# Kernel tuning notes

Measured on AMD Instinct MI355X. Metric: run time of the kernel, lower is better.

The kernel has to match this reference:

```python
import jax, jax.numpy as jnp
import numpy as np

QUALITY = 95
X_MIN, X_MAX = 0.0, 1.0

# JPEG Annex K base quantization tables
_LUMA = np.array([
    [16, 11, 10, 16, 24, 40, 51, 61],
    [12, 12, 14, 19, 26, 58, 60, 55],
    [14, 13, 16, 24, 40, 57, 69, 56],
    [14, 17, 22, 29, 51, 87, 80, 62],
    [18, 22, 37, 56, 68, 109, 103, 77],
    [24, 35, 55, 64, 81, 104, 113, 92],
    [49, 64, 78, 87, 103, 121, 120, 101],
    [72, 92, 95, 98, 112, 100, 103, 99]], dtype=np.float32)
_CHROMA = np.array([
    [17, 18, 24, 47, 99, 99, 99, 99],
    [18, 21, 26, 66, 99, 99, 99, 99],
    [24, 26, 56, 99, 99, 99, 99, 99],
    [47, 66, 99, 99, 99, 99, 99, 99],
    [99, 99, 99, 99, 99, 99, 99, 99],
    [99, 99, 99, 99, 99, 99, 99, 99],
    [99, 99, 99, 99, 99, 99, 99, 99],
    [99, 99, 99, 99, 99, 99, 99, 99]], dtype=np.float32)

def _qtable(base, quality):
    # libjpeg quality scaling (quality >= 50 branch)
    scale = 5000.0 / quality if quality < 50 else 200.0 - 2.0 * quality
    return np.clip(np.floor((base * scale + 50.0) / 100.0), 1.0, 255.0).astype(np.float32)

_QL = jnp.asarray(_qtable(_LUMA, QUALITY))
_QC = jnp.asarray(_qtable(_CHROMA, QUALITY))

# Orthonormal 8x8 DCT-II matrix
_k = np.arange(8)
_D = np.sqrt(2.0 / 8.0) * np.cos((2 * _k[None, :] + 1) * _k[:, None] * np.pi / 16.0)
_D[0, :] /= np.sqrt(2.0)
_D = jnp.asarray(_D.astype(np.float32))

def _jpeg_channel(ch, table):
    """8x8 block DCT -> quantize(round) -> dequantize -> IDCT. ch: [B,H,W] level-shifted."""
    B, H, W = ch.shape
    xb = ch.reshape(B, H // 8, 8, W // 8, 8)
    coef = jnp.einsum('ki,bhiwj,lj->bhkwl', _D, xb, _D)
    t = table[None, None, :, None, :]
    deq = jnp.round(coef / t) * t
    rec = jnp.einsum('ki,bhkwl,lj->bhiwj', _D, deq, _D)
    return rec.reshape(B, H, W)

def _jpeg_roundtrip(x255):
    """x255: [B,H,W,3] float values in [0,255]. Simulates JPEG encode+decode (4:2:0)."""
    r, g, b = x255[..., 0], x255[..., 1], x255[..., 2]
    # JFIF RGB -> YCbCr
    y = 0.299 * r + 0.587 * g + 0.114 * b
    cb = -0.168736 * r - 0.331264 * g + 0.5 * b + 128.0
    cr = 0.5 * r - 0.418688 * g - 0.081312 * b + 128.0
    # Luma at full resolution
    y2 = _jpeg_channel(y - 128.0, _QL) + 128.0
    # Chroma: 2x2 average downsample (4:2:0), codec, nearest upsample
    def down(c):
        B, H, W = c.shape
        return c.reshape(B, H // 2, 2, W // 2, 2).mean(axis=(2, 4))
    def up(c):
        return jnp.repeat(jnp.repeat(c, 2, axis=1), 2, axis=2)
    cb2 = up(_jpeg_channel(down(cb) - 128.0, _QC) + 128.0)
    cr2 = up(_jpeg_channel(down(cr) - 128.0, _QC) + 128.0)
    # YCbCr -> RGB
    r2 = y2 + 1.402 * (cr2 - 128.0)
    g2 = y2 - 0.344136 * (cb2 - 128.0) - 0.714136 * (cr2 - 128.0)
    b2 = y2 + 1.772 * (cb2 - 128.0)
    rgb = jnp.stack([r2, g2, b2], axis=-1)
    return jnp.round(jnp.clip(rgb, 0.0, 255.0))  # decoded uint8 values


def setup_inputs() -> dict:
    key = jax.random.key(0)
    x = jax.random.uniform(key, (32, 512, 512, 3), dtype=jnp.float32)
    return {"x": x}


def reference(x):
    # inputs -> uint8 pixel values (tf.cast truncation; values are >= 0)
    x255 = jnp.clip(jnp.floor((x - X_MIN) / ((X_MAX - X_MIN) / 255.0)), 0.0, 255.0)
    dec = _jpeg_roundtrip(x255)
    # back to input range/dtype
    return dec / (255.0 / (X_MAX - X_MIN)) + X_MIN
```

## Files before the change

### kernel.cpp

```cpp
#include <hip/hip_runtime.h>
#include <cstddef>

static constexpr float D8[8][8] = {
  { 0.35355339059327373f, 0.35355339059327373f, 0.35355339059327373f, 0.35355339059327373f,
    0.35355339059327373f, 0.35355339059327373f, 0.35355339059327373f, 0.35355339059327373f},
  { 0.4903926402016152f,  0.4157348061512726f,  0.27778511650980114f, 0.09754516100806417f,
   -0.09754516100806417f,-0.27778511650980114f,-0.4157348061512726f, -0.4903926402016152f},
  { 0.46193976625564337f, 0.19134171618254492f,-0.19134171618254492f,-0.46193976625564337f,
   -0.46193976625564337f,-0.19134171618254492f, 0.19134171618254492f, 0.46193976625564337f},
  { 0.4157348061512726f, -0.09754516100806417f,-0.4903926402016152f, -0.27778511650980114f,
    0.27778511650980114f, 0.4903926402016152f,  0.09754516100806417f,-0.4157348061512726f},
  { 0.35355339059327373f,-0.35355339059327373f,-0.35355339059327373f, 0.35355339059327373f,
    0.35355339059327373f,-0.35355339059327373f,-0.35355339059327373f, 0.35355339059327373f},
  { 0.27778511650980114f,-0.4903926402016152f,  0.09754516100806417f, 0.4157348061512726f,
   -0.4157348061512726f, -0.09754516100806417f, 0.4903926402016152f, -0.27778511650980114f},
  { 0.19134171618254492f,-0.46193976625564337f, 0.46193976625564337f,-0.19134171618254492f,
   -0.19134171618254492f, 0.46193976625564337f,-0.46193976625564337f, 0.19134171618254492f},
  { 0.09754516100806417f,-0.27778511650980114f, 0.4157348061512726f, -0.4903926402016152f,
    0.4903926402016152f, -0.4157348061512726f,  0.27778511650980114f,-0.09754516100806417f},
};

static constexpr float QLt[8][8] = {
  {2,1,1,2,2,4,5,6},
  {1,1,1,2,3,6,6,6},
  {1,1,2,2,4,6,7,6},
  {1,2,2,3,5,9,8,6},
  {2,2,4,6,7,11,10,8},
  {2,4,6,6,8,10,11,9},
  {5,6,8,9,10,12,12,10},
  {7,9,10,10,11,10,10,10},
};
static constexpr float QCt[8][8] = {
  {2,2,2,5,10,10,10,10},
  {2,2,3,7,10,10,10,10},
  {2,3,6,10,10,10,10,10},
  {5,7,10,10,10,10,10,10},
  {10,10,10,10,10,10,10,10},
  {10,10,10,10,10,10,10,10},
  {10,10,10,10,10,10,10,10},
  {10,10,10,10,10,10,10,10},
};

static constexpr float C255  = (float)(1.0/255.0);
static constexpr float RC255 = 1.0f / C255;

__device__ __forceinline__ float exact_div(float x, float c, float r) {
  float q0 = x * r;
  float e  = fmaf(-c, q0, x);
  return fmaf(e, r, q0);
}

__device__ __forceinline__ void dct8(const float x[8], float u[8]) {
  #pragma unroll
  for (int k = 0; k < 8; ++k) {
    float a = D8[k][0] * x[0];
    #pragma unroll
    for (int j = 1; j < 8; ++j) a += D8[k][j] * x[j];
    u[k] = a;
  }
}

__device__ __forceinline__ void idct8(const float x[8], float u[8]) {
  #pragma unroll
  for (int j = 0; j < 8; ++j) {
    float a = x[0] * D8[0][j];
    #pragma unroll
    for (int m = 1; m < 8; ++m) a += x[m] * D8[m][j];
    u[j] = a;
  }
}

__device__ __forceinline__ void xpose3(float a[8], float b[8], float c[8], int lane) {
  #pragma unroll
  for (int s = 1; s < 8; s <<= 1) {
    const bool hi = (lane & s) != 0;
    #pragma unroll
    for (int r0 = 0; r0 < 8; ++r0) {
      if (r0 & s) continue;
      const int r1 = r0 | s;
      const float a0 = a[r0], a1 = a[r1];
      const float b0 = b[r0], b1 = b[r1];
      const float c0 = c[r0], c1 = c[r1];
      const float ga = __shfl_xor(hi ? a0 : a1, s, 64);
      const float gb = __shfl_xor(hi ? b0 : b1, s, 64);
      const float gc = __shfl_xor(hi ? c0 : c1, s, 64);
      a[r0] = hi ? ga : a0;  a[r1] = hi ? a1 : ga;
      b[r0] = hi ? gb : b0;  b[r1] = hi ? b1 : gb;
      c[r0] = hi ? gc : c0;  c[r1] = hi ? c1 : gc;
    }
  }
}

__device__ __forceinline__ void quant8(float v[8], const float* QT, const float* RQ) {
  float4 Q0 = *(const float4*)&QT[0];
  float4 Q1 = *(const float4*)&QT[4];
  float4 R0 = *(const float4*)&RQ[0];
  float4 R1 = *(const float4*)&RQ[4];
  float qv[8] = {Q0.x,Q0.y,Q0.z,Q0.w,Q1.x,Q1.y,Q1.z,Q1.w};
  float rv[8] = {R0.x,R0.y,R0.z,R0.w,R1.x,R1.y,R1.z,R1.w};
  #pragma unroll
  for (int m = 0; m < 8; ++m)
    v[m] = rintf(exact_div(v[m], qv[m], rv[m])) * qv[m];
}

__global__ __launch_bounds__(64, 4) void jpeg_rt(const float* __restrict__ in,
                                                 float* __restrict__ out)
{
  __shared__ __align__(16) float Cbp[8][36];
  __shared__ __align__(16) float Crp[8][36];
  __shared__ __align__(16) float QTs[2][8][8];
  __shared__ __align__(16) float RQs[2][8][8];

  const int t   = threadIdx.x;
  const int g   = t >> 3;
  const int l   = t & 7;
  const int tx  = blockIdx.x;
  const int ty  = blockIdx.y;
  const int img = blockIdx.z;

  {
    const int i = t >> 3, m = t & 7;
    #pragma unroll
    for (int pl = 0; pl < 2; ++pl) {
      const float q = pl ? QCt[m][i] : QLt[m][i];
      QTs[pl][i][m] = q;
      RQs[pl][i][m] = 1.0f / q;
    }
  }

  const size_t imgbase = (size_t)img * (512*512);
  const int col0 = tx*64 + g*8;

  float vA[8], vB[8];

  #pragma unroll
  for (int rr = 0; rr < 2; ++rr) {
    const int r = l + rr*8;
    const float* rp = in + (imgbase + (size_t)(ty*16 + r)*512 + col0)*3;
    float4 P0 = ((const float4*)rp)[0];
    float4 P1 = ((const float4*)rp)[1];
    float4 P2 = ((const float4*)rp)[2];
    float4 P3 = ((const float4*)rp)[3];
    float4 P4 = ((const float4*)rp)[4];
    float4 P5 = ((const float4*)rp)[5];
    float px[24] = {P0.x,P0.y,P0.z,P0.w,P1.x,P1.y,P1.z,P1.w,
                    P2.x,P2.y,P2.z,P2.w,P3.x,P3.y,P3.z,P3.w,
                    P4.x,P4.y,P4.z,P4.w,P5.x,P5.y,P5.z,P5.w};
    float yv[8], cbv[8], crv[8];
    #pragma unroll
    for (int p = 0; p < 8; ++p) {
      float rc = fminf(fmaxf(floorf(exact_div(px[3*p+0], C255, RC255)), 0.0f), 255.0f);
      float gc = fminf(fmaxf(floorf(exact_div(px[3*p+1], C255, RC255)), 0.0f), 255.0f);
      float bc = fminf(fmaxf(floorf(exact_div(px[3*p+2], C255, RC255)), 0.0f), 255.0f);
      float y  =  0.299f*rc + 0.587f*gc + 0.114f*bc;
      float cb = -0.168736f*rc - 0.331264f*gc + 0.5f*bc + 128.0f;
      float cr =  0.5f*rc - 0.418688f*gc - 0.081312f*bc + 128.0f;
      yv[p]  = y - 128.0f;
      cbv[p] = cb;
      crv[p] = cr;
    }
    float hcb[4], hcr[4];
    #pragma unroll
    for (int k = 0; k < 4; ++k) {
      hcb[k] = cbv[2*k] + cbv[2*k+1];
      hcr[k] = crv[2*k] + crv[2*k+1];
    }
    float ocb[4], ocr[4];
    #pragma unroll
    for (int k = 0; k < 4; ++k) {
      ocb[k] = __shfl_xor(hcb[k], 1, 64);
      ocr[k] = __shfl_xor(hcr[k], 1, 64);
    }
    if ((l & 1) == 0) {
      const int crow = r >> 1;
      *(float4*)&Cbp[crow][g*4] = make_float4(
        (hcb[0]+ocb[0])*0.25f - 128.0f, (hcb[1]+ocb[1])*0.25f - 128.0f,
        (hcb[2]+ocb[2])*0.25f - 128.0f, (hcb[3]+ocb[3])*0.25f - 128.0f);
      *(float4*)&Crp[crow][g*4] = make_float4(
        (hcr[0]+ocr[0])*0.25f - 128.0f, (hcr[1]+ocr[1])*0.25f - 128.0f,
        (hcr[2]+ocr[2])*0.25f - 128.0f, (hcr[3]+ocr[3])*0.25f - 128.0f);
    }
    #pragma unroll
    for (int p = 0; p < 8; ++p) {
      if (rr == 0) vA[p] = yv[p]; else vB[p] = yv[p];
    }
  }
  __syncthreads();

  {
    float* plane = (g & 4) ? &Crp[0][0] : &Cbp[0][0];
    float* rowp  = plane + l*36 + (g & 3)*8;
    float4 L0 = *(const float4*)&rowp[0];
    float4 L1 = *(const float4*)&rowp[4];
    float vC[8] = {L0.x,L0.y,L0.z,L0.w,L1.x,L1.y,L1.z,L1.w};
    float uA[8], uB[8], uC[8];
    dct8(vA, uA); dct8(vB, uB); dct8(vC, uC);
    xpose3(uA, uB, uC, l);
    dct8(uA, vA); quant8(vA, &QTs[0][l][0], &RQs[0][l][0]);
    dct8(uB, vB); quant8(vB, &QTs[0][l][0], &RQs[0][l][0]);
    dct8(uC, vC); quant8(vC, &QTs[1][l][0], &RQs[1][l][0]);
    idct8(vA, uA); idct8(vB, uB); idct8(vC, uC);
    xpose3(uA, uB, uC, l);
    idct8(uA, vA); idct8(uB, vB); idct8(uC, vC);
    *(float4*)&rowp[0] = make_float4(vC[0],vC[1],vC[2],vC[3]);
    *(float4*)&rowp[4] = make_float4(vC[4],vC[5],vC[6],vC[7]);
  }
  __syncthreads();

  #pragma unroll
  for (int rr = 0; rr < 2; ++rr) {
    const int r = l + rr*8;
    const int crow = r >> 1;
    float4 CbF = *(const float4*)&Cbp[crow][g*4];
    float4 CrF = *(const float4*)&Crp[crow][g*4];
    float cbq[4] = {CbF.x,CbF.y,CbF.z,CbF.w};
    float crq[4] = {CrF.x,CrF.y,CrF.z,CrF.w};
    float ov[24];
    #pragma unroll
    for (int p = 0; p < 8; ++p) {
      float y2  = (rr ? vB[p] : vA[p]) + 128.0f;
      float cb2 = cbq[p>>1] + 128.0f;
      float cr2 = crq[p>>1] + 128.0f;
      float r2 = y2 + 1.402f*(cr2 - 128.0f);
      float g2 = y2 - 0.344136f*(cb2 - 128.0f) - 0.714136f*(cr2 - 128.0f);
      float b2 = y2 + 1.772f*(cb2 - 128.0f);
      ov[3*p+0] = exact_div(rintf(fminf(fmaxf(r2, 0.0f), 255.0f)), 255.0f, C255);
      ov[3*p+1] = exact_div(rintf(fminf(fmaxf(g2, 0.0f), 255.0f)), 255.0f, C255);
      ov[3*p+2] = exact_div(rintf(fminf(fmaxf(b2, 0.0f), 255.0f)), 255.0f, C255);
    }
    float* op = out + (imgbase + (size_t)(ty*16 + r)*512 + col0)*3;
    ((float4*)op)[0] = make_float4(ov[0], ov[1], ov[2], ov[3]);
    ((float4*)op)[1] = make_float4(ov[4], ov[5], ov[6], ov[7]);
    ((float4*)op)[2] = make_float4(ov[8], ov[9], ov[10],ov[11]);
    ((float4*)op)[3] = make_float4(ov[12],ov[13],ov[14],ov[15]);
    ((float4*)op)[4] = make_float4(ov[16],ov[17],ov[18],ov[19]);
    ((float4*)op)[5] = make_float4(ov[20],ov[21],ov[22],ov[23]);
  }
}

extern "C" void kernel_launch(void* const* d_in, const int* in_sizes, int n_in,
                              void* d_out, int out_size, void* d_ws, size_t ws_size,
                              hipStream_t stream) {
  (void)in_sizes; (void)n_in; (void)d_ws; (void)ws_size; (void)out_size;
  const float* x = (const float*)d_in[0];
  float* out = (float*)d_out;
  dim3 grid(8, 32, 32);
  jpeg_rt<<<grid, dim3(64), 0, stream>>>(x, out);
}
```

Measured before the change: 191.5 us.

## Process two row tiles per wave with prefetched loads overlapping compute

Each workgroup now has two waves, and each wave handles two 16-row tiles in sequence. The next tile's global row loads are issued before the DCT and output phases of the current tile, so memory latency overlaps compute. Plain __syncthreads is replaced by a raw LDS waitcnt plus s_barrier, and there are 4x fewer blocks. In exchange, the prefetched Row24 values raise register pressure, which may lower occupancy, and there is less block-level parallelism.

```diff
diff --git a/kernel.cpp b/kernel.cpp
--- a/kernel.cpp
+++ b/kernel.cpp
@@ -103,116 +103,81 @@
     v[m] = rintf(exact_div(v[m], qv[m], rv[m])) * qv[m];
 }
 
-__global__ __launch_bounds__(64, 4) void jpeg_rt(const float* __restrict__ in,
-                                                 float* __restrict__ out)
-{
-  __shared__ __align__(16) float Cbp[8][36];
-  __shared__ __align__(16) float Crp[8][36];
-  __shared__ __align__(16) float QTs[2][8][8];
-  __shared__ __align__(16) float RQs[2][8][8];
-
-  const int t   = threadIdx.x;
-  const int g   = t >> 3;
-  const int l   = t & 7;
-  const int tx  = blockIdx.x;
-  const int ty  = blockIdx.y;
-  const int img = blockIdx.z;
-
-  {
-    const int i = t >> 3, m = t & 7;
-    #pragma unroll
-    for (int pl = 0; pl < 2; ++pl) {
-      const float q = pl ? QCt[m][i] : QLt[m][i];
-      QTs[pl][i][m] = q;
-      RQs[pl][i][m] = 1.0f / q;
-    }
-  }
-
-  const size_t imgbase = (size_t)img * (512*512);
-  const int col0 = tx*64 + g*8;
-
-  float vA[8], vB[8];
-
-  #pragma unroll
-  for (int rr = 0; rr < 2; ++rr) {
-    const int r = l + rr*8;
-    const float* rp = in + (imgbase + (size_t)(ty*16 + r)*512 + col0)*3;
-    float4 P0 = ((const float4*)rp)[0];
-    float4 P1 = ((const float4*)rp)[1];
-    float4 P2 = ((const float4*)rp)[2];
-    float4 P3 = ((const float4*)rp)[3];
-    float4 P4 = ((const float4*)rp)[4];
-    float4 P5 = ((const float4*)rp)[5];
-    float px[24] = {P0.x,P0.y,P0.z,P0.w,P1.x,P1.y,P1.z,P1.w,
-                    P2.x,P2.y,P2.z,P2.w,P3.x,P3.y,P3.z,P3.w,
-                    P4.x,P4.y,P4.z,P4.w,P5.x,P5.y,P5.z,P5.w};
-    float yv[8], cbv[8], crv[8];
-    #pragma unroll
-    for (int p = 0; p < 8; ++p) {
-      float rc = fminf(fmaxf(floorf(exact_div(px[3*p+0], C255, RC255)), 0.0f), 255.0f);
-      float gc = fminf(fmaxf(floorf(exact_div(px[3*p+1], C255, RC255)), 0.0f), 255.0f);
-      float bc = fminf(fmaxf(floorf(exact_div(px[3*p+2], C255, RC255)), 0.0f), 255.0f);
-      float y  =  0.299f*rc + 0.587f*gc + 0.114f*bc;
-      float cb = -0.168736f*rc - 0.331264f*gc + 0.5f*bc + 128.0f;
-      float cr =  0.5f*rc - 0.418688f*gc - 0.081312f*bc + 128.0f;
-      yv[p]  = y - 128.0f;
-      cbv[p] = cb;
-      crv[p] = cr;
-    }
-    float hcb[4], hcr[4];
-    #pragma unroll
-    for (int k = 0; k < 4; ++k) {
-      hcb[k] = cbv[2*k] + cbv[2*k+1];
-      hcr[k] = crv[2*k] + crv[2*k+1];
-    }
-    float ocb[4], ocr[4];
-    #pragma unroll
-    for (int k = 0; k < 4; ++k) {
-      ocb[k] = __shfl_xor(hcb[k], 1, 64);
-      ocr[k] = __shfl_xor(hcr[k], 1, 64);
-    }
-    if ((l & 1) == 0) {
-      const int crow = r >> 1;
-      *(float4*)&Cbp[crow][g*4] = make_float4(
-        (hcb[0]+ocb[0])*0.25f - 128.0f, (hcb[1]+ocb[1])*0.25f - 128.0f,
-        (hcb[2]+ocb[2])*0.25f - 128.0f, (hcb[3]+ocb[3])*0.25f - 128.0f);
-      *(float4*)&Crp[crow][g*4] = make_float4(
-        (hcr[0]+ocr[0])*0.25f - 128.0f, (hcr[1]+ocr[1])*0.25f - 128.0f,
-        (hcr[2]+ocr[2])*0.25f - 128.0f, (hcr[3]+ocr[3])*0.25f - 128.0f);
-    }
-    #pragma unroll
-    for (int p = 0; p < 8; ++p) {
-      if (rr == 0) vA[p] = yv[p]; else vB[p] = yv[p];
-    }
-  }
-  __syncthreads();
-
-  {
-    float* plane = (g & 4) ? &Crp[0][0] : &Cbp[0][0];
-    float* rowp  = plane + l*36 + (g & 3)*8;
-    float4 L0 = *(const float4*)&rowp[0];
-    float4 L1 = *(const float4*)&rowp[4];
-    float vC[8] = {L0.x,L0.y,L0.z,L0.w,L1.x,L1.y,L1.z,L1.w};
-    float uA[8], uB[8], uC[8];
-    dct8(vA, uA); dct8(vB, uB); dct8(vC, uC);
-    xpose3(uA, uB, uC, l);
-    dct8(uA, vA); quant8(vA, &QTs[0][l][0], &RQs[0][l][0]);
-    dct8(uB, vB); quant8(vB, &QTs[0][l][0], &RQs[0][l][0]);
-    dct8(uC, vC); quant8(vC, &QTs[1][l][0], &RQs[1][l][0]);
-    idct8(vA, uA); idct8(vB, uB); idct8(vC, uC);
-    xpose3(uA, uB, uC, l);
-    idct8(uA, vA); idct8(uB, vB); idct8(uC, vC);
-    *(float4*)&rowp[0] = make_float4(vC[0],vC[1],vC[2],vC[3]);
-    *(float4*)&rowp[4] = make_float4(vC[4],vC[5],vC[6],vC[7]);
-  }
-  __syncthreads();
-
+#define WGBAR() do { \
+    asm volatile("s_waitcnt lgkmcnt(0)" ::: "memory"); \
+    __builtin_amdgcn_s_barrier(); \
+  } while (0)
+
+struct Row24 { float4 a, b, c, d, e, f; };
+
+__device__ __forceinline__ Row24 loadrow(const float* __restrict__ p) {
+  const float4* q = (const float4*)p;
+  Row24 r;
+  r.a = q[0]; r.b = q[1]; r.c = q[2]; r.d = q[3]; r.e = q[4]; r.f = q[5];
+  return r;
+}
+
+__device__ __forceinline__ void convert_row(const Row24& R, float yv[8],
+                                            float cbds[4], float crds[4]) {
+  float px[24] = {R.a.x,R.a.y,R.a.z,R.a.w, R.b.x,R.b.y,R.b.z,R.b.w,
+                  R.c.x,R.c.y,R.c.z,R.c.w, R.d.x,R.d.y,R.d.z,R.d.w,
+                  R.e.x,R.e.y,R.e.z,R.e.w, R.f.x,R.f.y,R.f.z,R.f.w};
+  float cbv[8], crv[8];
+  #pragma unroll
+  for (int p = 0; p < 8; ++p) {
+    float rc = fminf(fmaxf(floorf(exact_div(px[3*p+0], C255, RC255)), 0.0f), 255.0f);
+    float gc = fminf(fmaxf(floorf(exact_div(px[3*p+1], C255, RC255)), 0.0f), 255.0f);
+    float bc = fminf(fmaxf(floorf(exact_div(px[3*p+2], C255, RC255)), 0.0f), 255.0f);
+    float y  =  0.299f*rc + 0.587f*gc + 0.114f*bc;
+    float cb = -0.168736f*rc - 0.331264f*gc + 0.5f*bc + 128.0f;
+    float cr =  0.5f*rc - 0.418688f*gc - 0.081312f*bc + 128.0f;
+    yv[p]  = y - 128.0f;
+    cbv[p] = cb;
+    crv[p] = cr;
+  }
+  #pragma unroll
+  for (int k = 0; k < 4; ++k) {
+    float hcb = cbv[2*k] + cbv[2*k+1];
+    float hcr = crv[2*k] + crv[2*k+1];
+    float ocb = __shfl_xor(hcb, 1, 64);
+    float ocr = __shfl_xor(hcr, 1, 64);
+    cbds[k] = (hcb + ocb)*0.25f - 128.0f;
+    crds[k] = (hcr + ocr)*0.25f - 128.0f;
+  }
+}
+
+__device__ __forceinline__ void phaseB(float vA[8], float vB[8], int g, int l,
+                                       float* CbT, float* CrT,
+                                       const float* QTl, const float* RQl,
+                                       const float* QTc, const float* RQc) {
+  float* rowp = ((g & 4) ? CrT : CbT) + l*36 + (g & 3)*8;
+  float4 L0 = *(const float4*)&rowp[0];
+  float4 L1 = *(const float4*)&rowp[4];
+  float vC[8] = {L0.x,L0.y,L0.z,L0.w,L1.x,L1.y,L1.z,L1.w};
+  float uA[8], uB[8], uC[8];
+  dct8(vA, uA); dct8(vB, uB); dct8(vC, uC);
+  xpose3(uA, uB, uC, l);
+  dct8(uA, vA); quant8(vA, QTl, RQl);
+  dct8(uB, vB); quant8(vB, QTl, RQl);
+  dct8(uC, vC); quant8(vC, QTc, RQc);
+  idct8(vA, uA); idct8(vB, uB); idct8(vC, uC);
+  xpose3(uA, uB, uC, l);
+  idct8(uA, vA); idct8(uB, vB); idct8(uC, vC);
+  *(float4*)&rowp[0] = make_float4(vC[0],vC[1],vC[2],vC[3]);
+  *(float4*)&rowp[4] = make_float4(vC[4],vC[5],vC[6],vC[7]);
+}
+
+__device__ __forceinline__ void outputTile(const float vA[8], const float vB[8],
+                                           int g, int l,
+                                           const float* CbT, const float* CrT,
+                                           float* __restrict__ out,
+                                           size_t imgbase, int row0, int col0) {
   #pragma unroll
   for (int rr = 0; rr < 2; ++rr) {
     const int r = l + rr*8;
     const int crow = r >> 1;
-    float4 CbF = *(const float4*)&Cbp[crow][g*4];
-    float4 CrF = *(const float4*)&Crp[crow][g*4];
+    float4 CbF = *(const float4*)&CbT[crow*36 + g*4];
+    float4 CrF = *(const float4*)&CrT[crow*36 + g*4];
     float cbq[4] = {CbF.x,CbF.y,CbF.z,CbF.w};
     float crq[4] = {CrF.x,CrF.y,CrF.z,CrF.w};
     float ov[24];
@@ -228,7 +193,7 @@
       ov[3*p+1] = exact_div(rintf(fminf(fmaxf(g2, 0.0f), 255.0f)), 255.0f, C255);
       ov[3*p+2] = exact_div(rintf(fminf(fmaxf(b2, 0.0f), 255.0f)), 255.0f, C255);
     }
-    float* op = out + (imgbase + (size_t)(ty*16 + r)*512 + col0)*3;
+    float* op = out + (imgbase + (size_t)(row0 + r)*512 + col0)*3;
     ((float4*)op)[0] = make_float4(ov[0], ov[1], ov[2], ov[3]);
     ((float4*)op)[1] = make_float4(ov[4], ov[5], ov[6], ov[7]);
     ((float4*)op)[2] = make_float4(ov[8], ov[9], ov[10],ov[11]);
@@ -238,12 +203,98 @@
   }
 }
 
+__global__ __launch_bounds__(128, 4) void jpeg_rt(const float* __restrict__ in,
+                                                  float* __restrict__ out)
+{
+  __shared__ __align__(16) float Cbp[2][2][8][36];
+  __shared__ __align__(16) float Crp[2][2][8][36];
+  __shared__ __align__(16) float QTs[2][8][8];
+  __shared__ __align__(16) float RQs[2][8][8];
+
+  const int t    = threadIdx.x;
+  const int w    = t >> 6;
+  const int lane = t & 63;
+  const int g    = lane >> 3;
+  const int l    = lane & 7;
+  const int tx   = blockIdx.x;
+  const int ty   = blockIdx.y;
+  const int img  = blockIdx.z;
+
+  {
+    const int pl = t >> 6, i = (t >> 3) & 7, m = t & 7;
+    const float q = pl ? QCt[m][i] : QLt[m][i];
+    QTs[pl][i][m] = q;
+    RQs[pl][i][m] = 1.0f / q;
+  }
+
+  const size_t imgbase = (size_t)img * (512*512);
+  const int col0 = tx*64 + g*8;
+  const int row0 = ty*64 + w*32;
+
+  const float* QTl = &QTs[0][l][0];
+  const float* RQl = &RQs[0][l][0];
+  const float* QTc = &QTs[1][l][0];
+  const float* RQc = &RQs[1][l][0];
+  float* Cb0 = &Cbp[w][0][0][0];  float* Cr0 = &Crp[w][0][0][0];
+  float* Cb1 = &Cbp[w][1][0][0];  float* Cr1 = &Crp[w][1][0][0];
+
+  Row24 R00 = loadrow(in + (imgbase + (size_t)(row0 + l    )*512 + col0)*3);
+  Row24 R01 = loadrow(in + (imgbase + (size_t)(row0 + l + 8)*512 + col0)*3);
+  float vA0[8], vB0[8];
+  {
+    float cb0[4], cr0[4], cb1[4], cr1[4];
+    convert_row(R00, vA0, cb0, cr0);
+    convert_row(R01, vB0, cb1, cr1);
+    if ((l & 1) == 0) {
+      const int c0 = (l >> 1)*36 + g*4;
+      const int c1 = ((l >> 1) + 4)*36 + g*4;
+      *(float4*)&Cb0[c0] = make_float4(cb0[0],cb0[1],cb0[2],cb0[3]);
+      *(float4*)&Cr0[c0] = make_float4(cr0[0],cr0[1],cr0[2],cr0[3]);
+      *(float4*)&Cb0[c1] = make_float4(cb1[0],cb1[1],cb1[2],cb1[3]);
+      *(float4*)&Cr0[c1] = make_float4(cr1[0],cr1[1],cr1[2],cr1[3]);
+    }
+  }
+  Row24 R10 = loadrow(in + (imgbase + (size_t)(row0 + 16 + l)*512 + col0)*3);
+
+  WGBAR();
+
+  phaseB(vA0, vB0, g, l, Cb0, Cr0, QTl, RQl, QTc, RQc);
+
+  Row24 R11 = loadrow(in + (imgbase + (size_t)(row0 + 24 + l)*512 + col0)*3);
+
+  WGBAR();
+
+  outputTile(vA0, vB0, g, l, Cb0, Cr0, out, imgbase, row0, col0);
+
+  float vA1[8], vB1[8];
+  {
+    float cb0[4], cr0[4], cb1[4], cr1[4];
+    convert_row(R10, vA1, cb0, cr0);
+    convert_row(R11, vB1, cb1, cr1);
+    if ((l & 1) == 0) {
+      const int c0 = (l >> 1)*36 + g*4;
+      const int c1 = ((l >> 1) + 4)*36 + g*4;
+      *(float4*)&Cb1[c0] = make_float4(cb0[0],cb0[1],cb0[2],cb0[3]);
+      *(float4*)&Cr1[c0] = make_float4(cr0[0],cr0[1],cr0[2],cr0[3]);
+      *(float4*)&Cb1[c1] = make_float4(cb1[0],cb1[1],cb1[2],cb1[3]);
+      *(float4*)&Cr1[c1] = make_float4(cr1[0],cr1[1],cr1[2],cr1[3]);
+    }
+  }
+  WGBAR();
+
+  phaseB(vA1, vB1, g, l, Cb1, Cr1, QTl, RQl, QTc, RQc);
+
+  WGBAR();
+
+  outputTile(vA1, vB1, g, l, Cb1, Cr1, out, imgbase, row0 + 16, col0);
+}
+
 extern "C" void kernel_launch(void* const* d_in, const int* in_sizes, int n_in,
                               void* d_out, int out_size, void* d_ws, size_t ws_size,
                               hipStream_t stream) {
   (void)in_sizes; (void)n_in; (void)d_ws; (void)ws_size; (void)out_size;
   const float* x = (const float*)d_in[0];
   float* out = (float*)d_out;
-  dim3 grid(8, 32, 32);
-  jpeg_rt<<<grid, dim3(64), 0, stream>>>(x, out);
-}
+  dim3 grid(8, 8, 32);
+  jpeg_rt<<<grid, dim3(128), 0, stream>>>(x, out);
+}
```

Result: slower. 195.4 us (+2.0%).
